# Performance work log

Hardware: AMD Instinct MI355X
Metric: run time of the kernel (lower is better)

Reference implementation:

```python
import jax, jax.numpy as jnp
import numpy as np

B, N, DIM = 2, 512, 512
HEADS, DIM_HEAD, MAX_LEN = 8, 64, 1024


def _skew(QEr):
    # pad last dim on the left by 1, reshape (n, n+1) -> (n+1, n), drop first row
    padded = jnp.pad(QEr, ((0, 0), (0, 0), (0, 0), (1, 0)))
    b, h, r, c = padded.shape
    return padded.reshape(b, h, c, r)[:, :, 1:, :]


def _fft_multiply_parallel(A, x):
    # A: [b,h,n,n] decay matrix; x: [b,h,n,d]
    b, h, n, d = x.shape
    # y = [last column of A, first row of A] -> [b,h,2n]
    y = jnp.concatenate([A[:, :, :, -1], A[:, :, 0, :]], axis=-1)
    v = jnp.concatenate([x, jnp.zeros_like(x)], axis=-2)  # zero-pad rows n -> 2n
    # Faithful to the original torch code: fftn over ALL axes (incl. batch/head),
    # then ifft over the LAST axis only, then slice back to n rows.
    H = jnp.fft.fftn(y)[:, :, :, None] * jnp.fft.fftn(v)
    return jnp.fft.ifft(H)[:, :, :n, :]


def _forward(x, Wq, Wk, Wv, Er):
    b, n, _ = x.shape

    def split_heads(t):
        return t.reshape(b, n, HEADS, DIM_HEAD).transpose(0, 2, 1, 3)  # [b,h,n,d]

    q = split_heads(x @ Wq)
    k = split_heads(x @ Wk)
    v = split_heads(x @ Wv)
    # global (Frobenius) norm over the full tensor, as torch.norm(t)
    q = q / jnp.linalg.norm(q)
    k = k / jnp.linalg.norm(k)
    q_ = jax.nn.elu(q)
    k_ = jax.nn.elu(k)

    Er_t = Er[MAX_LEN - n:, :].T        # [d, n]
    QEr = q @ Er_t                       # [b,h,n,n]
    c = jnp.exp(_skew(QEr))              # relative-position decay, [b,h,n,n]

    a_1 = jnp.einsum('bhnx,bhny->bhnxy', k_, v).reshape(b, HEADS, n, DIM_HEAD * DIM_HEAD)
    d_2 = _fft_multiply_parallel(c, k_)                                   # [b,h,n,d] complex
    d_1 = _fft_multiply_parallel(c, a_1).reshape(b, HEADS, n, DIM_HEAD, DIM_HEAD)

    top = jnp.einsum('bhnx,bhnyz->bhnz', q_, d_1)    # complex [b,h,n,d]
    bottom = jnp.einsum('bhnx,bhny->bhny', q_, d_2)  # complex [b,h,n,d]
    return top / bottom


def setup_inputs() -> dict:
    key = jax.random.key(0)
    k1, k2, k3, k4, k5 = jax.random.split(key, 5)
    s = jnp.float32(1.0 / np.sqrt(DIM))
    return {
        'x': jax.random.normal(k1, (B, N, DIM), dtype=jnp.float32),
        'Wq': jax.random.normal(k2, (DIM, HEADS * DIM_HEAD), dtype=jnp.float32) * s,
        'Wk': jax.random.normal(k3, (DIM, HEADS * DIM_HEAD), dtype=jnp.float32) * s,
        'Wv': jax.random.normal(k4, (DIM, HEADS * DIM_HEAD), dtype=jnp.float32) * s,
        'Er': jax.random.normal(k5, (MAX_LEN, DIM_HEAD), dtype=jnp.float32),
    }


def reference(x, Wq, Wk, Wv, Er):
    return _forward(x, Wq, Wk, Wv, Er)
```

## Files before the change

### kernel.cpp

```cpp
#include <hip/hip_runtime.h>
#include <math.h>


#define DIMX 512
#define NPOS 512
#define PADIDX(m) ((m) + ((m) >> 4))

__global__ __launch_bounds__(256)
void gemm_kv_kernel(const float* __restrict__ x,
                    const float* __restrict__ Wk,
                    const float* __restrict__ Wv,
                    float* __restrict__ K,
                    float* __restrict__ V,
                    float* __restrict__ partials)
{
    const int blk  = blockIdx.x;
    const int sel  = blk >> 7;
    const int tid  = blk & 127;
    const int row0 = (tid >> 2) * 32;
    const int col0 = (tid & 3) * 128;
    const int t    = threadIdx.x;
    const int tc   = t & 31;
    const int tr   = t >> 5;
    const float* __restrict__ W   = sel ? Wv : Wk;
    float* __restrict__       Out = sel ? V  : K;

    __shared__ float xs[2][32][33];
    __shared__ float ws[2][32][128];
    __shared__ float red[4];

    float acc[4][4] = {{0,0,0,0},{0,0,0,0},{0,0,0,0},{0,0,0,0}};
    float  xr[4];
    float4 wv4[4];

    #define LD_GLOBAL(kb)                                                      \
        {   _Pragma("unroll")                                                  \
            for (int j = 0; j < 4; ++j) {                                      \
                const int idx = t + j * 256;                                   \
                xr[j] = x[(size_t)(row0 + (idx >> 5)) * DIMX + (kb) + (idx & 31)]; \
            }                                                                  \
            _Pragma("unroll")                                                  \
            for (int j = 0; j < 4; ++j) {                                      \
                const int f4 = t + j * 256;                                    \
                const int kk = f4 >> 5, cp = (f4 & 31) * 4;                    \
                wv4[j] = *(const float4*)&W[(size_t)((kb) + kk) * DIMX + col0 + cp]; \
            } }

    #define ST_LDS(buf)                                                        \
        {   _Pragma("unroll")                                                  \
            for (int j = 0; j < 4; ++j) {                                      \
                const int idx = t + j * 256;                                   \
                xs[buf][idx >> 5][idx & 31] = xr[j];                           \
            }                                                                  \
            _Pragma("unroll")                                                  \
            for (int j = 0; j < 4; ++j) {                                      \
                const int f4 = t + j * 256;                                    \
                const int kk = f4 >> 5, cp = (f4 & 31) * 4;                    \
                *(float4*)&ws[buf][kk][cp] = wv4[j];                           \
            } }

    LD_GLOBAL(0)
    ST_LDS(0)
    __syncthreads();

    for (int kb = 0; kb < 16; ++kb) {
        const int cur = kb & 1;
        if (kb < 15) LD_GLOBAL((kb + 1) * 32)
        #pragma unroll
        for (int kk = 0; kk < 32; ++kk) {
            const float4 w4 = *(const float4*)&ws[cur][kk][tc * 4];
            float xv[4];
            #pragma unroll
            for (int i = 0; i < 4; ++i) xv[i] = xs[cur][tr * 4 + i][kk];
            #pragma unroll
            for (int i = 0; i < 4; ++i) {
                acc[i][0] = fmaf(xv[i], w4.x, acc[i][0]);
                acc[i][1] = fmaf(xv[i], w4.y, acc[i][1]);
                acc[i][2] = fmaf(xv[i], w4.z, acc[i][2]);
                acc[i][3] = fmaf(xv[i], w4.w, acc[i][3]);
            }
        }
        if (kb < 15) {
            __syncthreads();
            ST_LDS(1 - cur)
            __syncthreads();
        }
    }

    float ss = 0.f;
    #pragma unroll
    for (int i = 0; i < 4; ++i) {
        const int row = row0 + tr * 4 + i;
        const float4 o = make_float4(acc[i][0], acc[i][1], acc[i][2], acc[i][3]);
        *(float4*)&Out[(size_t)row * DIMX + col0 + tc * 4] = o;
        ss += o.x * o.x + o.y * o.y + o.z * o.z + o.w * o.w;
    }
    if (sel == 0) {
        #pragma unroll
        for (int off = 32; off > 0; off >>= 1)
            ss += __shfl_down(ss, off, 64);
        if ((t & 63) == 0) red[t >> 6] = ss;
        __syncthreads();
        if (t == 0) partials[blk] = red[0] + red[1] + red[2] + red[3];
    } else {
        if (t == 0) partials[blk] = 0.f;
    }
    #undef LD_GLOBAL
    #undef ST_LDS
}

__device__ __constant__ float C8[8] = {
    1.f, 0.70710678118654752440f, 0.f, -0.70710678118654752440f,
   -1.f, -0.70710678118654752440f, 0.f, 0.70710678118654752440f };
__device__ __constant__ float S8[8] = {
    0.f, -0.70710678118654752440f, -1.f, -0.70710678118654752440f,
    0.f,  0.70710678118654752440f,  1.f,  0.70710678118654752440f };

__global__ __launch_bounds__(256)
void stage1_kernel(const float* __restrict__ K,
                   const float* __restrict__ V,
                   const float* __restrict__ partials,
                   float2* __restrict__ Gk,
                   float2* __restrict__ Gp)
{
    const int m = blockIdx.x;
    const int t = threadIdx.x;
    __shared__ float kk[2][8][64];
    __shared__ float pp[2][8][64];
    __shared__ float skp[16][4];
    __shared__ float sk[2][8];
    __shared__ float sred[4];

    float p = partials[t];
    #pragma unroll
    for (int off = 32; off > 0; off >>= 1)
        p += __shfl_down(p, off, 64);
    if ((t & 63) == 0) sred[t >> 6] = p;
    __syncthreads();
    const float scale = (float)(1.0 / sqrt((double)sred[0] + (double)sred[1] +
                                           (double)sred[2] + (double)sred[3]));

    for (int e = t; e < 1024; e += 256) {
        const int b = e >> 9, rem = e & 511, h = rem >> 6, z = rem & 63;
        const size_t src = (size_t)(b * 512 + m) * DIMX + h * 64 + z;
        const float kv = K[src] * scale;
        kk[b][h][z] = kv > 0.f ? kv : expm1f(kv);
        pp[b][h][z] = V[src];
    }
    __syncthreads();
    if (t < 64) {
        const int bh = t >> 2, q = t & 3;
        float s = 0.f;
        #pragma unroll
        for (int zz = 0; zz < 16; ++zz) s += kk[bh >> 3][bh & 7][q * 16 + zz];
        skp[bh][q] = s;
    }
    __syncthreads();
    if (t < 16) sk[t >> 3][t & 7] = skp[t][0] + skp[t][1] + skp[t][2] + skp[t][3];
    __syncthreads();
    for (int e = t; e < 1024; e += 256) {
        const int b = e >> 9, rem = e & 511, h = rem >> 6, z = rem & 63;
        pp[b][h][z] *= sk[b][h];
    }
    __syncthreads();

    for (int e2 = t; e2 < 512; e2 += 256) {
        const int be = e2 >> 5;
        const int zp = e2 & 31;
        const int beta = be >> 3, eta = be & 7;
        float4 rk, rp;
        #pragma unroll
        for (int zz = 0; zz < 2; ++zz) {
            const int z = zp * 2 + zz;
            float gkr = 0.f, gki = 0.f, gpr = 0.f, gpi = 0.f;
            #pragma unroll
            for (int b = 0; b < 2; ++b) {
                const float sgn = (beta & b) ? -1.f : 1.f;
                #pragma unroll
                for (int h = 0; h < 8; ++h) {
                    const int ph = (eta * h) & 7;
                    const float cr = C8[ph], ci = S8[ph];
                    const float a = kk[b][h][z] * sgn;
                    gkr = fmaf(a, cr, gkr); gki = fmaf(a, ci, gki);
                    const float p2 = pp[b][h][z] * sgn;
                    gpr = fmaf(p2, cr, gpr); gpi = fmaf(p2, ci, gpi);
                }
            }
            if (zz == 0) { rk.x = gkr; rk.y = gki; rp.x = gpr; rp.y = gpi; }
            else         { rk.z = gkr; rk.w = gki; rp.z = gpr; rp.w = gpi; }
        }
        const size_t o = ((size_t)be * NPOS + m) * 64 + zp * 2;
        *(float4*)&Gk[o] = rk;
        *(float4*)&Gp[o] = rp;
    }
}

__global__ __launch_bounds__(256)
void fft_div_kernel(const float2* __restrict__ Gk,
                    const float2* __restrict__ Gp,
                    float* __restrict__ out, int out_cplx)
{
    const int blk = blockIdx.x;
    const int j  = blk & 7;
    const int l  = (blk >> 3) & 3;
    const int be = blk >> 5;
    const int zg = j * 4 + l;
    const int t  = threadIdx.x;

    __shared__ float2 g[4][1088];
    __shared__ float2 w[544];

    for (int jj = t; jj < 512; jj += 256) {
        double s, cc;
        sincos(-6.2831853071795864769 * (double)jj / 1024.0, &s, &cc);
        w[PADIDX(jj)] = make_float2((float)cc, (float)s);
    }
    __syncthreads();

    for (int e = t; e < 1024; e += 256) {
        const int a = e >> 9;
        const int m = e & 511;
        const float4 v4 = *(const float4*)&(a ? Gp : Gk)[((size_t)be * NPOS + m) * 64 + zg * 2];
        const float2 v0 = make_float2(v4.x, v4.y);
        const float2 v1 = make_float2(v4.z, v4.w);
        const float2 tw = w[PADIDX(m)];
        g[a * 2 + 0][PADIDX(m)] = v0;
        g[a * 2 + 1][PADIDX(m)] = v1;
        g[a * 2 + 0][PADIDX(m + 512)] = make_float2(v0.x * tw.x - v0.y * tw.y,
                                                    v0.x * tw.y + v0.y * tw.x);
        g[a * 2 + 1][PADIDX(m + 512)] = make_float2(v1.x * tw.x - v1.y * tw.y,
                                                    v1.x * tw.y + v1.y * tw.x);
    }
    __syncthreads();

    #pragma unroll
    for (int s = 1; s <= 9; ++s) {
        const int S = 512 >> s;
        const int lg = 9 - s;
        #pragma unroll
        for (int q = 0; q < 8; ++q) {
            const int B    = t + 256 * q;
            const int arr  = B >> 9;
            const int beta = B & 511;
            const int jb   = beta & (S - 1);
            const int seg  = beta >> lg;
            const int u    = (seg << (lg + 1)) + jb;
            const int v    = u + S;
            const float2 tw = w[PADIDX(jb << s)];
            const float2 A  = g[arr][PADIDX(u)];
            const float2 Bb = g[arr][PADIDX(v)];
            g[arr][PADIDX(u)] = make_float2(A.x + Bb.x, A.y + Bb.y);
            const float sr = A.x - Bb.x, si = A.y - Bb.y;
            g[arr][PADIDX(v)] = make_float2(sr * tw.x - si * tw.y,
                                            sr * tw.y + si * tw.x);
        }
        __syncthreads();
    }

    for (int e2 = t; e2 < 512; e2 += 256) {
        const int i  = e2;
        const int pi = PADIDX(2 * i);
        const int mu = (int)(__brev((unsigned)i) >> 23);
        float4 res;
        #pragma unroll
        for (int zi = 0; zi < 2; ++zi) {
            const float2 D  = g[zi][pi];
            const float2 Nm = g[2 + zi][pi];
            const float inv = 1.f / (D.x * D.x + D.y * D.y);
            const float rr = (Nm.x * D.x + Nm.y * D.y) * inv;
            const float ri = (Nm.y * D.x - Nm.x * D.y) * inv;
            if (zi == 0) { res.x = rr; res.y = ri; }
            else         { res.z = rr; res.w = ri; }
        }
        const size_t o = ((size_t)be * NPOS + mu) * 64 + zg * 2;
        if (out_cplx) {
            *(float4*)&((float2*)out)[o] = res;
        } else {
            out[o]     = res.x;
            out[o + 1] = res.z;
        }
    }
}

__global__ __launch_bounds__(256)
void mdft_fallback_kernel(const float2* __restrict__ Gk,
                          const float2* __restrict__ Gp,
                          float* __restrict__ out,
                          int out_cplx)
{
    const int blk = blockIdx.x;
    const int be = blk >> 6, z = blk & 63;
    const int t = threadIdx.x;
    __shared__ float2 gk[512];
    __shared__ float2 gp[512];
    __shared__ float2 w[1024];

    for (int m = t; m < 512; m += 256) {
        const size_t idx = ((size_t)be * NPOS + m) * 64 + z;
        gk[m] = Gk[idx];
        gp[m] = Gp[idx];
    }
    for (int jj = t; jj < 1024; jj += 256) {
        double s, c;
        sincos(-6.2831853071795864769 * (double)jj / 1024.0, &s, &c);
        w[jj] = make_float2((float)c, (float)s);
    }
    __syncthreads();

    #pragma unroll
    for (int half = 0; half < 2; ++half) {
        const int mu = t + half * 256;
        double dr = 0.0, di = 0.0, nr = 0.0, ni = 0.0;
        int idx = 0;
        for (int m = 0; m < 512; ++m) {
            const float2 tw = w[idx];
            idx = (idx + mu) & 1023;
            const float2 a = gk[m];
            dr += (double)(a.x * tw.x - a.y * tw.y);
            di += (double)(a.x * tw.y + a.y * tw.x);
            const float2 p = gp[m];
            nr += (double)(p.x * tw.x - p.y * tw.y);
            ni += (double)(p.x * tw.y + p.y * tw.x);
        }
        const double dmag = dr * dr + di * di;
        const double orr = (nr * dr + ni * di) / dmag;
        const double oii = (ni * dr - nr * di) / dmag;
        const size_t o = ((size_t)be * NPOS + mu) * 64 + z;
        if (out_cplx) {
            out[2 * o]     = (float)orr;
            out[2 * o + 1] = (float)oii;
        } else {
            out[o] = (float)orr;
        }
    }
}

extern "C" void kernel_launch(void* const* d_in, const int* in_sizes, int n_in,
                              void* d_out, int out_size, void* d_ws, size_t ws_size,
                              hipStream_t stream)
{
    const float* x  = (const float*)d_in[0];
    const float* Wk = (const float*)d_in[2];
    const float* Wv = (const float*)d_in[3];
    float* out = (float*)d_out;

    char* ws = (char*)d_ws;
    float*  K    = (float*)(ws);
    float*  V    = (float*)(ws + (size_t)2097152);
    float2* Gk   = (float2*)(ws + (size_t)4194304);
    float*  part = (float*)(ws + (size_t)8388608);
    const int out_cplx = (out_size >= 2 * 2 * 8 * 512 * 64) ? 1 : 0;

    const bool ws_big = (ws_size >= (size_t)8390656 + (size_t)4194304);
    float2* Gp = ws_big ? (float2*)(ws + (size_t)8390656)
                        : (float2*)d_out;

    hipLaunchKernelGGL(gemm_kv_kernel, dim3(256), dim3(256), 0, stream,
                       x, Wk, Wv, K, V, part);
    hipLaunchKernelGGL(stage1_kernel, dim3(512), dim3(256), 0, stream,
                       K, V, part, Gk, Gp);
    if (ws_big) {
        hipLaunchKernelGGL(fft_div_kernel, dim3(512), dim3(256), 0, stream,
                           Gk, Gp, out, out_cplx);
    } else {
        hipLaunchKernelGGL(mdft_fallback_kernel, dim3(1024), dim3(256), 0, stream,
                           Gk, Gp, out, out_cplx);
    }
}
```

Before: 116.5 us.

## Stage full x row-block in LDS and stream W directly from global

New measurement: 122.2 us. 1.05x slower.

```diff
diff --git a/kernel.cpp b/kernel.cpp
--- a/kernel.cpp
+++ b/kernel.cpp
@@ -25,65 +25,47 @@
     const float* __restrict__ W   = sel ? Wv : Wk;
     float* __restrict__       Out = sel ? V  : K;
 
-    __shared__ float xs[2][32][33];
-    __shared__ float ws[2][32][128];
+    __shared__ float xs[32][DIMX];
     __shared__ float red[4];
 
+    for (int e = t * 4; e < 32 * DIMX; e += 1024) {
+        const int row = e >> 9, k = e & 511;
+        *(float4*)&xs[row][k] = *(const float4*)&x[(size_t)(row0 + row) * DIMX + k];
+    }
+    __syncthreads();
+
     float acc[4][4] = {{0,0,0,0},{0,0,0,0},{0,0,0,0},{0,0,0,0}};
-    float  xr[4];
-    float4 wv4[4];
-
-    #define LD_GLOBAL(kb)                                                      \
-        {   _Pragma("unroll")                                                  \
-            for (int j = 0; j < 4; ++j) {                                      \
-                const int idx = t + j * 256;                                   \
-                xr[j] = x[(size_t)(row0 + (idx >> 5)) * DIMX + (kb) + (idx & 31)]; \
-            }                                                                  \
-            _Pragma("unroll")                                                  \
-            for (int j = 0; j < 4; ++j) {                                      \
-                const int f4 = t + j * 256;                                    \
-                const int kk = f4 >> 5, cp = (f4 & 31) * 4;                    \
-                wv4[j] = *(const float4*)&W[(size_t)((kb) + kk) * DIMX + col0 + cp]; \
-            } }
-
-    #define ST_LDS(buf)                                                        \
-        {   _Pragma("unroll")                                                  \
-            for (int j = 0; j < 4; ++j) {                                      \
-                const int idx = t + j * 256;                                   \
-                xs[buf][idx >> 5][idx & 31] = xr[j];                           \
-            }                                                                  \
-            _Pragma("unroll")                                                  \
-            for (int j = 0; j < 4; ++j) {                                      \
-                const int f4 = t + j * 256;                                    \
-                const int kk = f4 >> 5, cp = (f4 & 31) * 4;                    \
-                *(float4*)&ws[buf][kk][cp] = wv4[j];                           \
-            } }
-
-    LD_GLOBAL(0)
-    ST_LDS(0)
-    __syncthreads();
-
-    for (int kb = 0; kb < 16; ++kb) {
-        const int cur = kb & 1;
-        if (kb < 15) LD_GLOBAL((kb + 1) * 32)
-        #pragma unroll
-        for (int kk = 0; kk < 32; ++kk) {
-            const float4 w4 = *(const float4*)&ws[cur][kk][tc * 4];
-            float xv[4];
+    const float* Wb = W + col0 + tc * 4;
+
+    float4 wnext[4];
+    #pragma unroll
+    for (int j = 0; j < 4; ++j)
+        wnext[j] = *(const float4*)&Wb[(size_t)j * DIMX];
+
+    for (int kb = 0; kb < 128; ++kb) {
+        float4 wcur[4];
+        #pragma unroll
+        for (int j = 0; j < 4; ++j) wcur[j] = wnext[j];
+        if (kb < 127) {
             #pragma unroll
-            for (int i = 0; i < 4; ++i) xv[i] = xs[cur][tr * 4 + i][kk];
+            for (int j = 0; j < 4; ++j)
+                wnext[j] = *(const float4*)&Wb[(size_t)((kb + 1) * 4 + j) * DIMX];
+        }
+        float4 xv[4];
+        #pragma unroll
+        for (int i = 0; i < 4; ++i)
+            xv[i] = *(const float4*)&xs[tr * 4 + i][kb * 4];
+        #pragma unroll
+        for (int i = 0; i < 4; ++i) {
             #pragma unroll
-            for (int i = 0; i < 4; ++i) {
-                acc[i][0] = fmaf(xv[i], w4.x, acc[i][0]);
-                acc[i][1] = fmaf(xv[i], w4.y, acc[i][1]);
-                acc[i][2] = fmaf(xv[i], w4.z, acc[i][2]);
-                acc[i][3] = fmaf(xv[i], w4.w, acc[i][3]);
+            for (int cc = 0; cc < 4; ++cc) {
+                float a = (&acc[i][0])[cc];
+                a = fmaf(xv[i].x, (&wcur[0].x)[cc], a);
+                a = fmaf(xv[i].y, (&wcur[1].x)[cc], a);
+                a = fmaf(xv[i].z, (&wcur[2].x)[cc], a);
+                a = fmaf(xv[i].w, (&wcur[3].x)[cc], a);
+                (&acc[i][0])[cc] = a;
             }
-        }
-        if (kb < 15) {
-            __syncthreads();
-            ST_LDS(1 - cur)
-            __syncthreads();
         }
     }
 
@@ -105,8 +87,6 @@
     } else {
         if (t == 0) partials[blk] = 0.f;
     }
-    #undef LD_GLOBAL
-    #undef ST_LDS
 }
 
 __device__ __constant__ float C8[8] = {
```
